# Performance work log

Measured on AMD Instinct MI355X. Metric: run time of the kernel, lower is better.

The kernel has to match this reference:

```python
import jax, jax.numpy as jnp
import numpy as np

N, IN_DIM, OUT_DIM = 8192, 512, 256
ALPHA = 0.2
NEG_INF = -9e15


def setup_inputs() -> dict:
    key = jax.random.key(0)
    k1, k2, k3, k4 = jax.random.split(key, 4)
    node_features = jax.random.normal(k1, (N, IN_DIM), dtype=jnp.float32)
    adj_matrix = jax.random.randint(k2, (N, N), 0, 2, dtype=jnp.int32)
    # xavier-uniform linear weight [out,in] -> store as [in,out]
    lim_w = float(np.sqrt(6.0 / (IN_DIM + OUT_DIM)))
    W = jax.random.uniform(k3, (IN_DIM, OUT_DIM), dtype=jnp.float32, minval=-lim_w, maxval=lim_w)
    b = jnp.zeros((OUT_DIM,), dtype=jnp.float32)
    # attention Linear(2*out_dim, 1): weight a [2*out_dim], bias scalar
    lim_a = float(np.sqrt(6.0 / (2 * OUT_DIM + 1)))
    a = jax.random.uniform(k4, (2 * OUT_DIM,), dtype=jnp.float32, minval=-lim_a, maxval=lim_a)
    a_bias = jnp.zeros((), dtype=jnp.float32)
    return {"adj_matrix": adj_matrix, "node_features": node_features, "W": W, "b": b, "a": a, "a_bias": a_bias}


def reference(adj_matrix, node_features, W, b, a, a_bias):
    # h = Linear(node_features); dropout is identity in eval mode
    h = node_features @ W + b                     # [N, D]
    # attention(cat(h_i, h_j)) == h_i @ a_l + h_j @ a_r + a_bias
    a_l, a_r = a[:OUT_DIM], a[OUT_DIM:]
    e_l = h @ a_l                                 # [N]
    e_r = h @ a_r                                 # [N]
    e = jax.nn.leaky_relu(e_l[:, None] + e_r[None, :] + a_bias, ALPHA)  # [N, N]
    scores = jnp.where(adj_matrix > 0, e, NEG_INF)
    attention = jax.nn.softmax(scores, axis=1)    # [N, N]
    h_prime = attention @ h                       # [N, D]
    return h_prime
```

## Files before the change

### kernel.cpp

```cpp
#include <hip/hip_runtime.h>

#define N 8192
#define DIN 512
#define DOUT 256
#define ALPHA 0.2f
#define NEG_INF -9.0e15f

typedef __attribute__((ext_vector_type(8))) short bf16x8;
typedef __attribute__((ext_vector_type(4))) float f32x4;
typedef __attribute__((ext_vector_type(4))) int   i32x4;

__device__ __forceinline__ unsigned f2bf_u(float f) {
    unsigned u = __builtin_bit_cast(unsigned, f);
    return (u + 0x7fffu + ((u >> 16) & 1u)) >> 16;
}
__device__ __forceinline__ unsigned pack2bf(float lo, float hi) {
    return f2bf_u(lo) | (f2bf_u(hi) << 16);
}
__device__ __forceinline__ float bf2f(ushort u) {
    return __builtin_bit_cast(float, (unsigned)u << 16);
}
union U4BF8 { uint4 u; bf16x8 v; };

__device__ __forceinline__ void async_copy16(const ushort* g, ushort* l) {
    __builtin_amdgcn_global_load_lds(
        (const __attribute__((address_space(1))) unsigned*)g,
        (__attribute__((address_space(3))) unsigned*)l, 16, 0, 0);
}

__global__ __launch_bounds__(256) void wb_kernel(const float* __restrict__ W,
                                                 ushort* __restrict__ WB) {
    const int g = blockIdx.x * 256 + threadIdx.x;
    const int c = g & 255, k8 = g >> 8;
    const float* wp = W + (size_t)(k8 * 8) * DOUT + c;
    U4BF8 o;
    o.u.x = pack2bf(wp[0 * DOUT], wp[1 * DOUT]);
    o.u.y = pack2bf(wp[2 * DOUT], wp[3 * DOUT]);
    o.u.z = pack2bf(wp[4 * DOUT], wp[5 * DOUT]);
    o.u.w = pack2bf(wp[6 * DOUT], wp[7 * DOUT]);
    *(uint4*)(WB + (size_t)g * 8) = o.u;
}

__global__ __launch_bounds__(256) void h_kernel(
        const float* __restrict__ X, const ushort* __restrict__ WB,
        const float* __restrict__ bvec, const float* __restrict__ a,
        ushort* __restrict__ hB, float* __restrict__ el, float* __restrict__ er)
{
    __shared__ float red[4][64][65];
    __shared__ float elr[2][4][16];
    const int t = threadIdx.x;
    const int w = t >> 6, l = t & 63, q = l >> 4, n = l & 15;
    const int i0 = blockIdx.x * 16;
    f32x4 acc[16];
    #pragma unroll
    for (int ct = 0; ct < 16; ++ct) acc[ct] = (f32x4){0.f, 0.f, 0.f, 0.f};
    const float* xp = X + (size_t)(i0 + n) * DIN + q * 8;

    #pragma unroll
    for (int ks = 0; ks < 4; ++ks) {
        const int k0 = w * 128 + ks * 32;
        const float4 x0 = *(const float4*)(xp + k0);
        const float4 x1 = *(const float4*)(xp + k0 + 4);
        U4BF8 pa;
        pa.u.x = pack2bf(x0.x, x0.y); pa.u.y = pack2bf(x0.z, x0.w);
        pa.u.z = pack2bf(x1.x, x1.y); pa.u.w = pack2bf(x1.z, x1.w);
        const ushort* wbp = WB + ((k0 >> 3) + q) * 2048 + n * 8;
        bf16x8 bfr[16];
        #pragma unroll
        for (int ct = 0; ct < 16; ++ct) bfr[ct] = *(const bf16x8*)(wbp + ct * 128);
        #pragma unroll
        for (int ct = 0; ct < 16; ++ct)
            acc[ct] = __builtin_amdgcn_mfma_f32_16x16x32_bf16(pa.v, bfr[ct], acc[ct], 0, 0, 0);
    }
    #pragma unroll
    for (int ct = 0; ct < 16; ++ct)
        #pragma unroll
        for (int r = 0; r < 4; ++r) red[w][l][ct * 4 + r] = acc[ct][r];
    __syncthreads();

    float pl[4] = {0.f, 0.f, 0.f, 0.f}, pr[4] = {0.f, 0.f, 0.f, 0.f};
    const int hbase = (blockIdx.x * 2 + (q >> 1)) * 2048 + n * 8 + (q & 1) * 4;
    #pragma unroll
    for (int c2 = 0; c2 < 4; ++c2) {
        const int ct = w * 4 + c2;
        const float bb = bvec[ct * 16 + n];
        const float al = a[ct * 16 + n];
        const float ar = a[DOUT + ct * 16 + n];
        float v[4];
        #pragma unroll
        for (int r = 0; r < 4; ++r) {
            v[r] = red[0][l][ct * 4 + r] + red[1][l][ct * 4 + r]
                 + red[2][l][ct * 4 + r] + red[3][l][ct * 4 + r] + bb;
            pl[r] += v[r] * al;
            pr[r] += v[r] * ar;
        }
        ushort4 hp;
        hp.x = (ushort)f2bf_u(v[0]); hp.y = (ushort)f2bf_u(v[1]);
        hp.z = (ushort)f2bf_u(v[2]); hp.w = (ushort)f2bf_u(v[3]);
        *(ushort4*)&hB[hbase + ct * 128] = hp;
    }
    #pragma unroll
    for (int r = 0; r < 4; ++r) {
        #pragma unroll
        for (int off = 1; off < 16; off <<= 1) {
            pl[r] += __shfl_xor(pl[r], off);
            pr[r] += __shfl_xor(pr[r], off);
        }
    }
    if (n == 0) {
        #pragma unroll
        for (int r = 0; r < 4; ++r) {
            elr[0][w][q * 4 + r] = pl[r];
            elr[1][w][q * 4 + r] = pr[r];
        }
    }
    __syncthreads();
    if (t < 16) {
        el[i0 + t] = elr[0][0][t] + elr[0][1][t] + elr[0][2][t] + elr[0][3][t];
        er[i0 + t] = elr[1][0][t] + elr[1][1][t] + elr[1][2][t] + elr[1][3][t];
    }
}

__global__ __launch_bounds__(512, 2) void attn_kernel(
        const int* __restrict__ adj, const float* __restrict__ el,
        const float* __restrict__ er, const float* __restrict__ ab,
        const ushort* __restrict__ hB, ushort* __restrict__ pout,
        float* __restrict__ plsum)
{
    __shared__ ushort stage[2][32768];
    __shared__ float ers[1024];
    const int t = threadIdx.x;
    const int w = t >> 6, l = t & 63, q = l >> 4, n = l & 15;
    const int rb = blockIdx.x >> 3, jq = blockIdx.x & 7;
    const int j0 = jq * 1024;
    const int rowA = rb * 256 + w * 32 + n;
    const float elmA = el[rowA] + ab[0];
    const float elmB = el[rowA + 16] + ab[0];
    const int* apA = adj + (size_t)rowA * N + j0 + q * 8;
    const int* apB = apA + (size_t)16 * N;

    f32x4 acc0[16], acc1[16];
    #pragma unroll
    for (int ct = 0; ct < 16; ++ct) {
        acc0[ct] = (f32x4){0.f, 0.f, 0.f, 0.f};
        acc1[ct] = (f32x4){0.f, 0.f, 0.f, 0.f};
    }
    float lsumA = 0.f, lsumB = 0.f;

    *(float2*)&ers[t * 2] = *(const float2*)&er[j0 + t * 2];
    i32x4 a[16];
    #pragma unroll
    for (int kg = 0; kg < 4; ++kg) {
        a[2 * kg]     = *(const i32x4*)(apA + kg * 32);
        a[2 * kg + 1] = *(const i32x4*)(apA + kg * 32 + 4);
        a[8 + 2 * kg] = *(const i32x4*)(apB + kg * 32);
        a[9 + 2 * kg] = *(const i32x4*)(apB + kg * 32 + 4);
    }
    {
        const ushort* g = hB + (size_t)j0 * 256 + t * 8;
        ushort* lb = &stage[0][t * 8];
        #pragma unroll
        for (int i = 0; i < 8; ++i) async_copy16(g + i * 4096, lb + i * 4096);
    }

    for (int s = 0; s < 8; ++s) {
        __syncthreads();
        U4BF8 paA[4], paB[4];
        #pragma unroll
        for (int kg = 0; kg < 4; ++kg) {
            const float4 e0 = *(const float4*)&ers[s * 128 + kg * 32 + q * 8];
            const float4 e1 = *(const float4*)&ers[s * 128 + kg * 32 + q * 8 + 4];
            float v, p0, p1, p2, p3, p4, p5, p6, p7;
            i32x4 a0 = a[2 * kg], a1 = a[2 * kg + 1];
            v = elmA + e0.x; v = fmaxf(v, ALPHA * v); p0 = __expf(a0.x > 0 ? v : NEG_INF);
            v = elmA + e0.y; v = fmaxf(v, ALPHA * v); p1 = __expf(a0.y > 0 ? v : NEG_INF);
            v = elmA + e0.z; v = fmaxf(v, ALPHA * v); p2 = __expf(a0.z > 0 ? v : NEG_INF);
            v = elmA + e0.w; v = fmaxf(v, ALPHA * v); p3 = __expf(a0.w > 0 ? v : NEG_INF);
            v = elmA + e1.x; v = fmaxf(v, ALPHA * v); p4 = __expf(a1.x > 0 ? v : NEG_INF);
            v = elmA + e1.y; v = fmaxf(v, ALPHA * v); p5 = __expf(a1.y > 0 ? v : NEG_INF);
            v = elmA + e1.z; v = fmaxf(v, ALPHA * v); p6 = __expf(a1.z > 0 ? v : NEG_INF);
            v = elmA + e1.w; v = fmaxf(v, ALPHA * v); p7 = __expf(a1.w > 0 ? v : NEG_INF);
            lsumA += p0 + p1 + p2 + p3 + p4 + p5 + p6 + p7;
            paA[kg].u.x = pack2bf(p0, p1); paA[kg].u.y = pack2bf(p2, p3);
            paA[kg].u.z = pack2bf(p4, p5); paA[kg].u.w = pack2bf(p6, p7);
            a0 = a[8 + 2 * kg]; a1 = a[9 + 2 * kg];
            v = elmB + e0.x; v = fmaxf(v, ALPHA * v); p0 = __expf(a0.x > 0 ? v : NEG_INF);
            v = elmB + e0.y; v = fmaxf(v, ALPHA * v); p1 = __expf(a0.y > 0 ? v : NEG_INF);
            v = elmB + e0.z; v = fmaxf(v, ALPHA * v); p2 = __expf(a0.z > 0 ? v : NEG_INF);
            v = elmB + e0.w; v = fmaxf(v, ALPHA * v); p3 = __expf(a0.w > 0 ? v : NEG_INF);
            v = elmB + e1.x; v = fmaxf(v, ALPHA * v); p4 = __expf(a1.x > 0 ? v : NEG_INF);
            v = elmB + e1.y; v = fmaxf(v, ALPHA * v); p5 = __expf(a1.y > 0 ? v : NEG_INF);
            v = elmB + e1.z; v = fmaxf(v, ALPHA * v); p6 = __expf(a1.z > 0 ? v : NEG_INF);
            v = elmB + e1.w; v = fmaxf(v, ALPHA * v); p7 = __expf(a1.w > 0 ? v : NEG_INF);
            lsumB += p0 + p1 + p2 + p3 + p4 + p5 + p6 + p7;
            paB[kg].u.x = pack2bf(p0, p1); paB[kg].u.y = pack2bf(p2, p3);
            paB[kg].u.z = pack2bf(p4, p5); paB[kg].u.w = pack2bf(p6, p7);
        }
        if (s < 7) {
            const int off = (s + 1) * 128;
            #pragma unroll
            for (int kg = 0; kg < 4; ++kg) {
                a[2 * kg]     = *(const i32x4*)(apA + off + kg * 32);
                a[2 * kg + 1] = *(const i32x4*)(apA + off + kg * 32 + 4);
                a[8 + 2 * kg] = *(const i32x4*)(apB + off + kg * 32);
                a[9 + 2 * kg] = *(const i32x4*)(apB + off + kg * 32 + 4);
            }
            const ushort* g = hB + (size_t)(j0 + off) * 256 + t * 8;
            ushort* lb = &stage[(s + 1) & 1][t * 8];
            #pragma unroll
            for (int i = 0; i < 8; ++i) async_copy16(g + i * 4096, lb + i * 4096);
        }
        #pragma unroll
        for (int kg = 0; kg < 4; ++kg) {
            const ushort* sb = &stage[s & 1][(kg * 4 + q) * 2048 + n * 8];
            #pragma unroll
            for (int ct = 0; ct < 16; ++ct) {
                const bf16x8 bf = *(const bf16x8*)(sb + ct * 128);
                acc0[ct] = __builtin_amdgcn_mfma_f32_16x16x32_bf16(paA[kg].v, bf, acc0[ct], 0, 0, 0);
                acc1[ct] = __builtin_amdgcn_mfma_f32_16x16x32_bf16(paB[kg].v, bf, acc1[ct], 0, 0, 0);
            }
        }
    }

    lsumA += __shfl_xor(lsumA, 16);
    lsumA += __shfl_xor(lsumA, 32);
    lsumB += __shfl_xor(lsumB, 16);
    lsumB += __shfl_xor(lsumB, 32);
    if (l < 16) {
        plsum[(size_t)jq * N + rowA] = lsumA;
        plsum[(size_t)jq * N + rowA + 16] = lsumB;
    }

    ushort* pb0 = pout + ((size_t)jq * N + rb * 256 + w * 32 + q * 4) * 256 + n;
    ushort* pb1 = pb0 + 16 * 256;
    #pragma unroll
    for (int ct = 0; ct < 16; ++ct)
        #pragma unroll
        for (int r = 0; r < 4; ++r) {
            __builtin_nontemporal_store((ushort)f2bf_u(acc0[ct][r]),
                                        pb0 + (size_t)r * 256 + ct * 16);
            __builtin_nontemporal_store((ushort)f2bf_u(acc1[ct][r]),
                                        pb1 + (size_t)r * 256 + ct * 16);
        }
}

__global__ __launch_bounds__(256) void combine_kernel(
        const ushort* __restrict__ pout, const float* __restrict__ plsum,
        float* __restrict__ out)
{
    const int t = threadIdx.x;
    const int row = blockIdx.x * 4 + (t >> 6);
    const int c = (t & 63) * 4;
    const size_t idx = (size_t)row * 256 + c;
    const size_t qs = (size_t)N * 256;
    float4 o = {0.f, 0.f, 0.f, 0.f};
    float ls = 0.f;
    #pragma unroll
    for (int p = 0; p < 8; ++p) {
        const ushort4 v = *(const ushort4*)&pout[idx + p * qs];
        o.x += bf2f(v.x); o.y += bf2f(v.y); o.z += bf2f(v.z); o.w += bf2f(v.w);
        ls += plsum[p * N + row];
    }
    const float li = 1.0f / ls;
    o.x *= li; o.y *= li; o.z *= li; o.w *= li;
    *(float4*)&out[idx] = o;
}

extern "C" void kernel_launch(void* const* d_in, const int* in_sizes, int n_in,
                              void* d_out, int out_size, void* d_ws, size_t ws_size,
                              hipStream_t stream) {
    const int*   adj = (const int*)  d_in[0];
    const float* X   = (const float*)d_in[1];
    const float* W   = (const float*)d_in[2];
    const float* b   = (const float*)d_in[3];
    const float* a   = (const float*)d_in[4];
    const float* ab  = (const float*)d_in[5];
    float* out = (float*)d_out;

    ushort* hB    = (ushort*)d_ws;
    ushort* WB    = hB + (size_t)N * DOUT;
    float*  el    = (float*)(WB + (size_t)DIN * DOUT);
    float*  er    = el + N;
    float*  plsum = er + N;
    ushort* pout  = (ushort*)(plsum + 8 * N);

    wb_kernel<<<dim3(64), dim3(256), 0, stream>>>(W, WB);
    h_kernel<<<dim3(N / 16), dim3(256), 0, stream>>>(X, WB, b, a, hB, el, er);
    attn_kernel<<<dim3(256), dim3(512), 0, stream>>>(adj, el, er, ab, hB, pout, plsum);
    combine_kernel<<<dim3(N / 4), dim3(256), 0, stream>>>(pout, plsum, out);
}
```

Measured before the change: 510.9 us.

## Pack adjacency into bitmask and vectorize partial-output stores with matching combine

Adds a pre-pass that converts the int32 adjacency into a per-row bitmask so the attention kernel loads one 32-bit word per step instead of sixteen int vectors, freeing registers. The attention kernel's partial outputs are now written as packed 16-byte bf16 vectors in the MFMA fragment layout, and the combine kernel is rewritten to read that layout and scatter to the final row-major output. The cost is an extra kernel launch that still streams the full adjacency, plus scattered scalar fp32 stores in combine.

```diff
diff --git a/kernel.cpp b/kernel.cpp
--- a/kernel.cpp
+++ b/kernel.cpp
@@ -17,8 +17,11 @@
 __device__ __forceinline__ unsigned pack2bf(float lo, float hi) {
     return f2bf_u(lo) | (f2bf_u(hi) << 16);
 }
-__device__ __forceinline__ float bf2f(ushort u) {
-    return __builtin_bit_cast(float, (unsigned)u << 16);
+__device__ __forceinline__ float bf2f_lo(unsigned u) {
+    return __builtin_bit_cast(float, u << 16);
+}
+__device__ __forceinline__ float bf2f_hi(unsigned u) {
+    return __builtin_bit_cast(float, u & 0xffff0000u);
 }
 union U4BF8 { uint4 u; bf16x8 v; };
 
@@ -41,6 +44,24 @@
     *(uint4*)(WB + (size_t)g * 8) = o.u;
 }
 
+__global__ __launch_bounds__(256) void pack_kernel(const int* __restrict__ adj,
+                                                   unsigned char* __restrict__ bits) {
+    const int t = threadIdx.x;
+    const int r = blockIdx.x * 16 + (t >> 4);
+    const int c = t & 15;
+    const int* ap = adj + (size_t)r * N + c * 8;
+    unsigned char* bp = bits + (size_t)r * (N / 8) + (c & 3) * 4 + (c >> 2);
+    for (int s = 0; s < 64; ++s) {
+        const i32x4 a0 = *(const i32x4*)(ap + s * 128);
+        const i32x4 a1 = *(const i32x4*)(ap + s * 128 + 4);
+        unsigned b = (a0.x > 0 ? 1u : 0u)  | (a0.y > 0 ? 2u : 0u)
+                   | (a0.z > 0 ? 4u : 0u)  | (a0.w > 0 ? 8u : 0u)
+                   | (a1.x > 0 ? 16u : 0u) | (a1.y > 0 ? 32u : 0u)
+                   | (a1.z > 0 ? 64u : 0u) | (a1.w > 0 ? 128u : 0u);
+        bp[s * 16] = (unsigned char)b;
+    }
+}
+
 __global__ __launch_bounds__(256) void h_kernel(
         const float* __restrict__ X, const ushort* __restrict__ WB,
         const float* __restrict__ bvec, const float* __restrict__ a,
@@ -121,8 +142,8 @@
     }
 }
 
-__global__ __launch_bounds__(512, 2) void attn_kernel(
-        const int* __restrict__ adj, const float* __restrict__ el,
+__global__ __launch_bounds__(512, 1) void attn_kernel(
+        const unsigned char* __restrict__ bits, const float* __restrict__ el,
         const float* __restrict__ er, const float* __restrict__ ab,
         const ushort* __restrict__ hB, ushort* __restrict__ pout,
         float* __restrict__ plsum)
@@ -136,8 +157,8 @@
     const int rowA = rb * 256 + w * 32 + n;
     const float elmA = el[rowA] + ab[0];
     const float elmB = el[rowA + 16] + ab[0];
-    const int* apA = adj + (size_t)rowA * N + j0 + q * 8;
-    const int* apB = apA + (size_t)16 * N;
+    const uint* mpA = (const uint*)(bits + (size_t)rowA * (N / 8) + jq * 128) + q;
+    const uint* mpB = (const uint*)(bits + (size_t)(rowA + 16) * (N / 8) + jq * 128) + q;
 
     f32x4 acc0[16], acc1[16];
     #pragma unroll
@@ -148,14 +169,7 @@
     float lsumA = 0.f, lsumB = 0.f;
 
     *(float2*)&ers[t * 2] = *(const float2*)&er[j0 + t * 2];
-    i32x4 a[16];
-    #pragma unroll
-    for (int kg = 0; kg < 4; ++kg) {
-        a[2 * kg]     = *(const i32x4*)(apA + kg * 32);
-        a[2 * kg + 1] = *(const i32x4*)(apA + kg * 32 + 4);
-        a[8 + 2 * kg] = *(const i32x4*)(apB + kg * 32);
-        a[9 + 2 * kg] = *(const i32x4*)(apB + kg * 32 + 4);
-    }
+    uint mA = mpA[0], mB = mpB[0];
     {
         const ushort* g = hB + (size_t)j0 * 256 + t * 8;
         ushort* lb = &stage[0][t * 8];
@@ -165,50 +179,45 @@
 
     for (int s = 0; s < 8; ++s) {
         __syncthreads();
+        const uint mmA = mA, mmB = mB;
+        if (s < 7) {
+            mA = mpA[(s + 1) * 4];
+            mB = mpB[(s + 1) * 4];
+            const ushort* g = hB + (size_t)(j0 + (s + 1) * 128) * 256 + t * 8;
+            ushort* lb = &stage[(s + 1) & 1][t * 8];
+            #pragma unroll
+            for (int i = 0; i < 8; ++i) async_copy16(g + i * 4096, lb + i * 4096);
+        }
         U4BF8 paA[4], paB[4];
         #pragma unroll
         for (int kg = 0; kg < 4; ++kg) {
+            const uint bkA = (mmA >> (kg * 8)) & 0xffu;
+            const uint bkB = (mmB >> (kg * 8)) & 0xffu;
             const float4 e0 = *(const float4*)&ers[s * 128 + kg * 32 + q * 8];
             const float4 e1 = *(const float4*)&ers[s * 128 + kg * 32 + q * 8 + 4];
             float v, p0, p1, p2, p3, p4, p5, p6, p7;
-            i32x4 a0 = a[2 * kg], a1 = a[2 * kg + 1];
-            v = elmA + e0.x; v = fmaxf(v, ALPHA * v); p0 = __expf(a0.x > 0 ? v : NEG_INF);
-            v = elmA + e0.y; v = fmaxf(v, ALPHA * v); p1 = __expf(a0.y > 0 ? v : NEG_INF);
-            v = elmA + e0.z; v = fmaxf(v, ALPHA * v); p2 = __expf(a0.z > 0 ? v : NEG_INF);
-            v = elmA + e0.w; v = fmaxf(v, ALPHA * v); p3 = __expf(a0.w > 0 ? v : NEG_INF);
-            v = elmA + e1.x; v = fmaxf(v, ALPHA * v); p4 = __expf(a1.x > 0 ? v : NEG_INF);
-            v = elmA + e1.y; v = fmaxf(v, ALPHA * v); p5 = __expf(a1.y > 0 ? v : NEG_INF);
-            v = elmA + e1.z; v = fmaxf(v, ALPHA * v); p6 = __expf(a1.z > 0 ? v : NEG_INF);
-            v = elmA + e1.w; v = fmaxf(v, ALPHA * v); p7 = __expf(a1.w > 0 ? v : NEG_INF);
+            v = elmA + e0.x; v = fmaxf(v, ALPHA * v); p0 = __expf(bkA & 1u   ? v : NEG_INF);
+            v = elmA + e0.y; v = fmaxf(v, ALPHA * v); p1 = __expf(bkA & 2u   ? v : NEG_INF);
+            v = elmA + e0.z; v = fmaxf(v, ALPHA * v); p2 = __expf(bkA & 4u   ? v : NEG_INF);
+            v = elmA + e0.w; v = fmaxf(v, ALPHA * v); p3 = __expf(bkA & 8u   ? v : NEG_INF);
+            v = elmA + e1.x; v = fmaxf(v, ALPHA * v); p4 = __expf(bkA & 16u  ? v : NEG_INF);
+            v = elmA + e1.y; v = fmaxf(v, ALPHA * v); p5 = __expf(bkA & 32u  ? v : NEG_INF);
+            v = elmA + e1.z; v = fmaxf(v, ALPHA * v); p6 = __expf(bkA & 64u  ? v : NEG_INF);
+            v = elmA + e1.w; v = fmaxf(v, ALPHA * v); p7 = __expf(bkA & 128u ? v : NEG_INF);
             lsumA += p0 + p1 + p2 + p3 + p4 + p5 + p6 + p7;
             paA[kg].u.x = pack2bf(p0, p1); paA[kg].u.y = pack2bf(p2, p3);
             paA[kg].u.z = pack2bf(p4, p5); paA[kg].u.w = pack2bf(p6, p7);
-            a0 = a[8 + 2 * kg]; a1 = a[9 + 2 * kg];
-            v = elmB + e0.x; v = fmaxf(v, ALPHA * v); p0 = __expf(a0.x > 0 ? v : NEG_INF);
-            v = elmB + e0.y; v = fmaxf(v, ALPHA * v); p1 = __expf(a0.y > 0 ? v : NEG_INF);
-            v = elmB + e0.z; v = fmaxf(v, ALPHA * v); p2 = __expf(a0.z > 0 ? v : NEG_INF);
-            v = elmB + e0.w; v = fmaxf(v, ALPHA * v); p3 = __expf(a0.w > 0 ? v : NEG_INF);
-            v = elmB + e1.x; v = fmaxf(v, ALPHA * v); p4 = __expf(a1.x > 0 ? v : NEG_INF);
-            v = elmB + e1.y; v = fmaxf(v, ALPHA * v); p5 = __expf(a1.y > 0 ? v : NEG_INF);
-            v = elmB + e1.z; v = fmaxf(v, ALPHA * v); p6 = __expf(a1.z > 0 ? v : NEG_INF);
-            v = elmB + e1.w; v = fmaxf(v, ALPHA * v); p7 = __expf(a1.w > 0 ? v : NEG_INF);
+            v = elmB + e0.x; v = fmaxf(v, ALPHA * v); p0 = __expf(bkB & 1u   ? v : NEG_INF);
+            v = elmB + e0.y; v = fmaxf(v, ALPHA * v); p1 = __expf(bkB & 2u   ? v : NEG_INF);
+            v = elmB + e0.z; v = fmaxf(v, ALPHA * v); p2 = __expf(bkB & 4u   ? v : NEG_INF);
+            v = elmB + e0.w; v = fmaxf(v, ALPHA * v); p3 = __expf(bkB & 8u   ? v : NEG_INF);
+            v = elmB + e1.x; v = fmaxf(v, ALPHA * v); p4 = __expf(bkB & 16u  ? v : NEG_INF);
+            v = elmB + e1.y; v = fmaxf(v, ALPHA * v); p5 = __expf(bkB & 32u  ? v : NEG_INF);
+            v = elmB + e1.z; v = fmaxf(v, ALPHA * v); p6 = __expf(bkB & 64u  ? v : NEG_INF);
+            v = elmB + e1.w; v = fmaxf(v, ALPHA * v); p7 = __expf(bkB & 128u ? v : NEG_INF);
             lsumB += p0 + p1 + p2 + p3 + p4 + p5 + p6 + p7;
             paB[kg].u.x = pack2bf(p0, p1); paB[kg].u.y = pack2bf(p2, p3);
             paB[kg].u.z = pack2bf(p4, p5); paB[kg].u.w = pack2bf(p6, p7);
-        }
-        if (s < 7) {
-            const int off = (s + 1) * 128;
-            #pragma unroll
-            for (int kg = 0; kg < 4; ++kg) {
-                a[2 * kg]     = *(const i32x4*)(apA + off + kg * 32);
-                a[2 * kg + 1] = *(const i32x4*)(apA + off + kg * 32 + 4);
-                a[8 + 2 * kg] = *(const i32x4*)(apB + off + kg * 32);
-                a[9 + 2 * kg] = *(const i32x4*)(apB + off + kg * 32 + 4);
-            }
-            const ushort* g = hB + (size_t)(j0 + off) * 256 + t * 8;
-            ushort* lb = &stage[(s + 1) & 1][t * 8];
-            #pragma unroll
-            for (int i = 0; i < 8; ++i) async_copy16(g + i * 4096, lb + i * 4096);
         }
         #pragma unroll
         for (int kg = 0; kg < 4; ++kg) {
@@ -231,39 +240,69 @@
         plsum[(size_t)jq * N + rowA + 16] = lsumB;
     }
 
-    ushort* pb0 = pout + ((size_t)jq * N + rb * 256 + w * 32 + q * 4) * 256 + n;
+    ushort* pb0 = pout + (size_t)jq * N * 256
+                + ((size_t)rb * 256 + w * 32) * 256 + l * 64;
     ushort* pb1 = pb0 + 16 * 256;
     #pragma unroll
-    for (int ct = 0; ct < 16; ++ct)
-        #pragma unroll
-        for (int r = 0; r < 4; ++r) {
-            __builtin_nontemporal_store((ushort)f2bf_u(acc0[ct][r]),
-                                        pb0 + (size_t)r * 256 + ct * 16);
-            __builtin_nontemporal_store((ushort)f2bf_u(acc1[ct][r]),
-                                        pb1 + (size_t)r * 256 + ct * 16);
-        }
+    for (int c2 = 0; c2 < 8; ++c2) {
+        uint4 o0, o1;
+        o0.x = pack2bf(acc0[2 * c2][0],     acc0[2 * c2][1]);
+        o0.y = pack2bf(acc0[2 * c2][2],     acc0[2 * c2][3]);
+        o0.z = pack2bf(acc0[2 * c2 + 1][0], acc0[2 * c2 + 1][1]);
+        o0.w = pack2bf(acc0[2 * c2 + 1][2], acc0[2 * c2 + 1][3]);
+        *(uint4*)(pb0 + c2 * 8) = o0;
+        o1.x = pack2bf(acc1[2 * c2][0],     acc1[2 * c2][1]);
+        o1.y = pack2bf(acc1[2 * c2][2],     acc1[2 * c2][3]);
+        o1.z = pack2bf(acc1[2 * c2 + 1][0], acc1[2 * c2 + 1][1]);
+        o1.w = pack2bf(acc1[2 * c2 + 1][2], acc1[2 * c2 + 1][3]);
+        *(uint4*)(pb1 + c2 * 8) = o1;
+    }
 }
 
 __global__ __launch_bounds__(256) void combine_kernel(
         const ushort* __restrict__ pout, const float* __restrict__ plsum,
         float* __restrict__ out)
 {
+    __shared__ float linv[16];
     const int t = threadIdx.x;
-    const int row = blockIdx.x * 4 + (t >> 6);
-    const int c = (t & 63) * 4;
-    const size_t idx = (size_t)row * 256 + c;
+    const int rg = blockIdx.x;
+    if (t < 16) {
+        float s = 0.f;
+        #pragma unroll
+        for (int p = 0; p < 8; ++p) s += plsum[p * N + rg * 16 + t];
+        linv[t] = 1.0f / s;
+    }
+    __syncthreads();
+
     const size_t qs = (size_t)N * 256;
-    float4 o = {0.f, 0.f, 0.f, 0.f};
-    float ls = 0.f;
+    const size_t base = (size_t)rg * 4096 + t * 16;
+    float v[16];
+    #pragma unroll
+    for (int i = 0; i < 16; ++i) v[i] = 0.f;
     #pragma unroll
     for (int p = 0; p < 8; ++p) {
-        const ushort4 v = *(const ushort4*)&pout[idx + p * qs];
-        o.x += bf2f(v.x); o.y += bf2f(v.y); o.z += bf2f(v.z); o.w += bf2f(v.w);
-        ls += plsum[p * N + row];
-    }
-    const float li = 1.0f / ls;
-    o.x *= li; o.y *= li; o.z *= li; o.w *= li;
-    *(float4*)&out[idx] = o;
+        const uint4 u0 = *(const uint4*)&pout[p * qs + base];
+        const uint4 u1 = *(const uint4*)&pout[p * qs + base + 8];
+        v[0]  += bf2f_lo(u0.x); v[1]  += bf2f_hi(u0.x);
+        v[2]  += bf2f_lo(u0.y); v[3]  += bf2f_hi(u0.y);
+        v[4]  += bf2f_lo(u0.z); v[5]  += bf2f_hi(u0.z);
+        v[6]  += bf2f_lo(u0.w); v[7]  += bf2f_hi(u0.w);
+        v[8]  += bf2f_lo(u1.x); v[9]  += bf2f_hi(u1.x);
+        v[10] += bf2f_lo(u1.y); v[11] += bf2f_hi(u1.y);
+        v[12] += bf2f_lo(u1.z); v[13] += bf2f_hi(u1.z);
+        v[14] += bf2f_lo(u1.w); v[15] += bf2f_hi(u1.w);
+    }
+    const int qn = t >> 2, ct4 = t & 3;
+    const int q = qn >> 4, n = qn & 15;
+    #pragma unroll
+    for (int cl = 0; cl < 4; ++cl) {
+        const int col = (ct4 * 4 + cl) * 16 + n;
+        #pragma unroll
+        for (int r = 0; r < 4; ++r) {
+            const int row = rg * 16 + q * 4 + r;
+            out[(size_t)row * 256 + col] = v[cl * 4 + r] * linv[q * 4 + r];
+        }
+    }
 }
 
 extern "C" void kernel_launch(void* const* d_in, const int* in_sizes, int n_in,
@@ -283,9 +322,11 @@
     float*  er    = el + N;
     float*  plsum = er + N;
     ushort* pout  = (ushort*)(plsum + 8 * N);
+    unsigned char* bits = (unsigned char*)(pout + (size_t)8 * N * DOUT);
 
     wb_kernel<<<dim3(64), dim3(256), 0, stream>>>(W, WB);
+    pack_kernel<<<dim3(N / 16), dim3(256), 0, stream>>>(adj, bits);
     h_kernel<<<dim3(N / 16), dim3(256), 0, stream>>>(X, WB, b, a, hB, el, er);
-    attn_kernel<<<dim3(256), dim3(512), 0, stream>>>(adj, el, er, ab, hB, pout, plsum);
-    combine_kernel<<<dim3(N / 4), dim3(256), 0, stream>>>(pout, plsum, out);
-}
+    attn_kernel<<<dim3(256), dim3(512), 0, stream>>>(bits, el, er, ab, hB, pout, plsum);
+    combine_kernel<<<dim3(N / 16), dim3(256), 0, stream>>>(pout, plsum, out);
+}
```

Result: faster. 448.0 us (-12.3%).
